# Performance work log

Measured on AMD Instinct MI355X. Metric: run time of the kernel, lower is better.

Reference implementation:

```python
import jax, jax.numpy as jnp
import numpy as np
import jax.scipy.linalg as jsl

N = 20000
E = 320000
IN_FEAT = 128
HID = 128
OUT_FEAT = 64
D = 4            # stalk_dim
K = HID // D     # number of stalks per node
MLP_HID = 64


def setup_inputs() -> dict:
    key = jax.random.key(0)
    ks = jax.random.split(key, 16)
    def lin(kw, kb, fan_in, fan_out):
        s = 1.0 / np.sqrt(fan_in)
        w = jax.random.uniform(kw, (fan_in, fan_out), minval=-s, maxval=s, dtype=jnp.float32)
        b = jax.random.uniform(kb, (fan_out,), minval=-s, maxval=s, dtype=jnp.float32)
        return w, b
    x = jax.random.normal(ks[0], (N, IN_FEAT), dtype=jnp.float32)
    edge_index = jax.random.randint(ks[1], (2, E), 0, N, dtype=jnp.int64)
    lin_in_w, lin_in_b = lin(ks[2], ks[3], IN_FEAT, HID)
    conv0_w1, conv0_b1 = lin(ks[4], ks[5], 2 * HID, MLP_HID)
    conv0_w2, conv0_b2 = lin(ks[6], ks[7], MLP_HID, 2 * D * D)
    conv1_w1, conv1_b1 = lin(ks[8], ks[9], 2 * HID, MLP_HID)
    conv1_w2, conv1_b2 = lin(ks[10], ks[11], MLP_HID, 2 * D * D)
    lin_out_w, lin_out_b = lin(ks[12], ks[13], HID, OUT_FEAT)
    return {
        "x": x, "edge_index": edge_index,
        "lin_in_w": lin_in_w, "lin_in_b": lin_in_b,
        "conv0_w1": conv0_w1, "conv0_b1": conv0_b1,
        "conv0_w2": conv0_w2, "conv0_b2": conv0_b2, "conv0_eps": jnp.float32(0.5),
        "conv1_w1": conv1_w1, "conv1_b1": conv1_b1,
        "conv1_w2": conv1_w2, "conv1_b2": conv1_b2, "conv1_eps": jnp.float32(0.5),
        "lin_out_w": lin_out_w, "lin_out_b": lin_out_b,
    }


def _sheaf_conv(x, row, col, w1, b1, w2, b2, eps):
    # edge gather -> MLP -> skew-symmetric expm -> batched small matmuls -> scatter-add
    x_row = x[row]              # [E, C] source features
    x_col = x[col]              # [E, C] target features
    h = jax.nn.relu(jnp.concatenate([x_row, x_col], axis=-1) @ w1 + b1)
    maps = (h @ w2 + b2).reshape(-1, 2, D, D)        # [E, 2, d, d]
    A = maps - jnp.swapaxes(maps, -1, -2)            # skew-symmetric
    F_e = jax.vmap(jsl.expm)(A.reshape(-1, D, D)).reshape(-1, 2, D, D)
    f_u, f_v = F_e[:, 0], F_e[:, 1]                  # [E, d, d] each
    # PyG default flow: x_i = x[col] (target), x_j = x[row] (source)
    x_i = x_col.reshape(-1, K, D)
    x_j = x_row.reshape(-1, K, D)
    proj_i = jnp.einsum('eab,ekb->eka', f_u, x_i)
    proj_j = jnp.einsum('eab,ekb->eka', f_v, x_j)
    err = proj_i - proj_j
    msg = jnp.einsum('eba,ekb->eka', f_u, err).reshape(-1, K * D)  # f_u^T @ err
    agg = jax.ops.segment_sum(msg, col, num_segments=x.shape[0])   # scatter-add at target
    return x - eps * agg


def reference(x, edge_index, lin_in_w, lin_in_b,
              conv0_w1, conv0_b1, conv0_w2, conv0_b2, conv0_eps,
              conv1_w1, conv1_b1, conv1_w2, conv1_b2, conv1_eps,
              lin_out_w, lin_out_b):
    row, col = edge_index[0], edge_index[1]
    h = x @ lin_in_w + lin_in_b
    h = jax.nn.elu(_sheaf_conv(h, row, col, conv0_w1, conv0_b1, conv0_w2, conv0_b2, conv0_eps))
    h = jax.nn.elu(_sheaf_conv(h, row, col, conv1_w1, conv1_b1, conv1_w2, conv1_b2, conv1_eps))
    return h @ lin_out_w + lin_out_b
```

## Files before the change

### kernel.cpp

```cpp
#include <hip/hip_runtime.h>
#include <math.h>


using short8 = __attribute__((ext_vector_type(8))) short;
using f32x4 = __attribute__((ext_vector_type(4))) float;
typedef unsigned short u16;

__device__ __forceinline__ u16 f2bf(float f) {
  unsigned u = __float_as_uint(f);
  unsigned r = (u + 0x7FFFu + ((u >> 16) & 1u)) >> 16;
  return (u16)r;
}
__device__ __forceinline__ float bf2f(u16 v) {
  return __uint_as_float(((unsigned)v) << 16);
}

__global__ void __launch_bounds__(256) k_prep(const float* __restrict__ x,
    u16* __restrict__ Xb, int* __restrict__ cnt, int n4, int N,
    const float* __restrict__ win, const float* __restrict__ w1a,
    const float* __restrict__ w1b, const float* __restrict__ wout,
    const float* __restrict__ w2a, const float* __restrict__ w2b,
    const float* __restrict__ b1a, const float* __restrict__ b1b,
    u16* __restrict__ WTin, u16* __restrict__ WT1a, u16* __restrict__ WT1b,
    u16* __restrict__ WTout, u16* __restrict__ W2Ta, u16* __restrict__ W2Tb,
    float* __restrict__ B1pa, float* __restrict__ B1pb) {
  int idx = blockIdx.x * 256 + threadIdx.x;
  if (idx < N) cnt[idx] = 0;
  if (idx < n4) {
    float4 v = ((const float4*)x)[idx];
    ushort4 o;
    o.x = f2bf(v.x);
    o.y = f2bf(v.y);
    o.z = f2bf(v.z);
    o.w = f2bf(v.w);
    ((ushort4*)Xb)[idx] = o;
  }
  if (idx < 16384) {
    int o = idx >> 7, i = idx & 127;
    WTin[idx] = f2bf(win[i * 128 + o]);
  } else if (idx < 32768) {
    int j = idx - 16384;
    int o = j >> 7, i = j & 127;
    WT1a[j] = f2bf(o < 64 ? w1a[i * 64 + o] : w1a[(128 + i) * 64 + (o - 64)]);
  } else if (idx < 49152) {
    int j = idx - 32768;
    int o = j >> 7, i = j & 127;
    WT1b[j] = f2bf(o < 64 ? w1b[i * 64 + o] : w1b[(128 + i) * 64 + (o - 64)]);
  } else if (idx < 57344) {
    int j = idx - 49152;
    int o = j >> 7, i = j & 127;
    WTout[j] = f2bf(wout[i * 64 + o]);
  } else if (idx < 59392) {
    int j = idx - 57344;
    int o = j >> 6, k = j & 63;
    W2Ta[j] = f2bf(w2a[k * 32 + o]);
  } else if (idx < 61440) {
    int j = idx - 59392;
    int o = j >> 6, k = j & 63;
    W2Tb[j] = f2bf(w2b[k * 32 + o]);
  } else if (idx < 61568) {
    int j = idx - 61440;
    B1pa[j] = (j < 64) ? 0.f : b1a[j - 64];
  } else if (idx < 61696) {
    int j = idx - 61568;
    B1pb[j] = (j < 64) ? 0.f : b1b[j - 64];
  }
}

__global__ void __launch_bounds__(256) k_gemm_mfma(const u16* __restrict__ Ab,
    const u16* __restrict__ WT, const float* __restrict__ bias,
    float* __restrict__ C, u16* __restrict__ Cb, int N, int P) {
  int t = threadIdx.x;
  int wv = t >> 6, lane = t & 63;
  int row0 = (blockIdx.x << 6) + (wv << 4);
  int cb = blockIdx.y << 4;
  int col = lane & 15, quad = lane >> 4;
  const u16* wrow = WT + (size_t)(cb + col) * 128 + quad * 8;
  short8 b0 = *(const short8*)(wrow);
  short8 b1 = *(const short8*)(wrow + 32);
  short8 b2 = *(const short8*)(wrow + 64);
  short8 b3 = *(const short8*)(wrow + 96);
  float bv = bias ? bias[cb + col] : 0.f;
  const u16* ar = Ab + (size_t)(row0 + col) * 128 + quad * 8;
  short8 a0 = *(const short8*)(ar);
  short8 a1 = *(const short8*)(ar + 32);
  short8 a2 = *(const short8*)(ar + 64);
  short8 a3 = *(const short8*)(ar + 96);
  f32x4 acc = {0.f, 0.f, 0.f, 0.f};
  acc = __builtin_amdgcn_mfma_f32_16x16x32_bf16(a0, b0, acc, 0, 0, 0);
  acc = __builtin_amdgcn_mfma_f32_16x16x32_bf16(a1, b1, acc, 0, 0, 0);
  acc = __builtin_amdgcn_mfma_f32_16x16x32_bf16(a2, b2, acc, 0, 0, 0);
  acc = __builtin_amdgcn_mfma_f32_16x16x32_bf16(a3, b3, acc, 0, 0, 0);
#pragma unroll
  for (int r = 0; r < 4; ++r) {
    int row = row0 + quad * 4 + r;
    if (row < N) {
      float o = acc[r] + bv;
      if (C) C[(size_t)row * P + cb + col] = o;
      if (Cb) Cb[(size_t)row * 128 + cb + col] = f2bf(o);
    }
  }
}

__global__ void __launch_bounds__(256) k_hist(const int* __restrict__ eidx,
                                              int* __restrict__ cnt, int E) {
  int e = blockIdx.x * 256 + threadIdx.x;
  if (e < E) atomicAdd(&cnt[eidx[E + e]], 1);
}

__global__ void __launch_bounds__(256) k_scanA(const int* __restrict__ cnt,
                                               int* __restrict__ bsum, int N) {
  __shared__ int sums[256];
  int b = blockIdx.x, t = threadIdx.x;
  int base = b * 2048 + t * 8;
  int s = 0;
#pragma unroll
  for (int k = 0; k < 8; ++k) {
    int i = base + k;
    if (i < N) s += cnt[i];
  }
  sums[t] = s;
  __syncthreads();
  for (int d = 128; d > 0; d >>= 1) {
    if (t < d) sums[t] += sums[t + d];
    __syncthreads();
  }
  if (t == 0) bsum[b] = sums[0];
}

__global__ void __launch_bounds__(256) k_scanC(const int* __restrict__ cnt,
    const int* __restrict__ bsum, int* __restrict__ ptr,
    int* __restrict__ cursor, int N, int nblocks) {
  __shared__ int sums[256];
  int b = blockIdx.x, t = threadIdx.x;
  int bo = 0;
  for (int k = 0; k < b; ++k) bo += bsum[k];
  int base = b * 2048 + t * 8;
  int vals[8];
  int s = 0;
#pragma unroll
  for (int k = 0; k < 8; ++k) {
    int i = base + k;
    int c = (i < N) ? cnt[i] : 0;
    vals[k] = s;
    s += c;
  }
  sums[t] = s;
  __syncthreads();
  for (int d = 1; d < 256; d <<= 1) {
    int v = (t >= d) ? sums[t - d] : 0;
    __syncthreads();
    sums[t] += v;
    __syncthreads();
  }
  int toff = (t == 0) ? 0 : sums[t - 1];
#pragma unroll
  for (int k = 0; k < 8; ++k) {
    int i = base + k;
    if (i < N) {
      int p = bo + toff + vals[k];
      ptr[i] = p;
      cursor[i] = p;
    }
  }
  if (b == nblocks - 1 && t == 255) ptr[N] = bo + sums[255];
}

__global__ void __launch_bounds__(256) k_fill(const int* __restrict__ eidx,
    int* __restrict__ cursor, int2* __restrict__ adj, int E) {
  int e = blockIdx.x * 256 + threadIdx.x;
  if (e >= E) return;
  int r = eidx[e], c = eidx[E + e];
  int pos = atomicAdd(&cursor[c], 1);
  adj[pos] = make_int2(r, c);
}

__device__ __forceinline__ void so4_expm(const float* __restrict__ m,
                                         float* __restrict__ F) {
  float v1 = m[1] - m[4], v2 = m[2] - m[8], v3 = m[3] - m[12];
  float w1 = m[11] - m[14], w2 = m[13] - m[7], w3 = m[6] - m[9];
  float p1 = 0.5f * (v1 + w1), p2 = 0.5f * (v2 + w2), p3 = 0.5f * (v3 + w3);
  float q1 = 0.5f * (v1 - w1), q2 = 0.5f * (v2 - w2), q3 = 0.5f * (v3 - w3);
  float tp2 = p1 * p1 + p2 * p2 + p3 * p3;
  float tq2 = q1 * q1 + q2 * q2 + q3 * q3;
  float tp = sqrtf(tp2), tq = sqrtf(tq2);
  float cp = __cosf(tp);
  float sp = (tp > 1e-6f) ? (__sinf(tp) / tp) : (1.f - tp2 * (1.f / 6.f));
  float cq = __cosf(tq);
  float sq = (tq > 1e-6f) ? (__sinf(tq) / tq) : (1.f - tq2 * (1.f / 6.f));
  float a1 = sp * p1, a2 = sp * p2, a3 = sp * p3;
  float b1 = sq * q1, b2 = sq * q2, b3 = sq * q3;
  float Rp[16] = {cp,  a1,  a2,  a3,  -a1, cp,  a3,  -a2,
                  -a2, -a3, cp,  a1,  -a3, a2,  -a1, cp};
  float Rq[16] = {cq,  b1,  b2,  b3,  -b1, cq,  -b3, b2,
                  -b2, b3,  cq,  -b1, -b3, -b2, b1,  cq};
#pragma unroll
  for (int a = 0; a < 4; ++a)
#pragma unroll
    for (int b = 0; b < 4; ++b) {
      float s = 0.f;
#pragma unroll
      for (int c = 0; c < 4; ++c) s = fmaf(Rp[a * 4 + c], Rq[c * 4 + b], s);
      F[a * 4 + b] = s;
    }
}

__global__ void __launch_bounds__(64) k_conv(const float* __restrict__ x,
    const u16* __restrict__ xgb, const u16* __restrict__ pqb,
    const u16* __restrict__ W2T, const float* __restrict__ b2,
    const int* __restrict__ ptr, const int2* __restrict__ adj,
    const float* __restrict__ epsp, float* __restrict__ xout,
    u16* __restrict__ xoutb, int N) {
  __shared__ float ms[16 * 44];
  int lane = threadIdx.x;
  int v = blockIdx.x;
  if (v >= N) return;
  int p0 = ptr[v], p1 = ptr[v + 1];
  int el = lane & 15, quad = lane >> 4;
  int a = lane & 3, kb = lane & ~3;
  short8 bf00 = *(const short8*)(W2T + (size_t)el * 64 + quad * 8);
  short8 bf01 = *(const short8*)(W2T + (size_t)el * 64 + 32 + quad * 8);
  short8 bf10 = *(const short8*)(W2T + (size_t)(16 + el) * 64 + quad * 8);
  short8 bf11 = *(const short8*)(W2T + (size_t)(16 + el) * 64 + 32 + quad * 8);
  float b2a = b2[el], b2b = b2[16 + el];
  short8 qv0 = *(const short8*)(pqb + (size_t)v * 128 + 64 + quad * 8);
  short8 qv1 = *(const short8*)(pqb + (size_t)v * 128 + 96 + quad * 8);
  const float* xv = x + (size_t)v * 128;
  float4 xi1 = *(const float4*)(xv + kb);
  float4 xi2 = *(const float4*)(xv + 64 + kb);
  float hv1 = xv[lane], hv2 = xv[64 + lane];
  float s10 = 0.f, s11 = 0.f, s12 = 0.f, s13 = 0.f;
  float acc1 = 0.f, acc2 = 0.f;
  for (int b0 = p0; b0 < p1; b0 += 16) {
    int nb = p1 - b0;
    nb = (nb > 16) ? 16 : nb;
    int ee = b0 + ((el < nb) ? el : (nb - 1));
    int row = adj[ee].x;
    f32x4 c0 = {0.f, 0.f, 0.f, 0.f};
    f32x4 c1 = {0.f, 0.f, 0.f, 0.f};
    {
      short8 pv = *(const short8*)(pqb + (size_t)row * 128 + quad * 8);
      short8 av;
#pragma unroll
      for (int j = 0; j < 8; ++j) {
        float h = bf2f((u16)pv[j]) + bf2f((u16)qv0[j]);
        av[j] = (short)f2bf(fmaxf(h, 0.f));
      }
      c0 = __builtin_amdgcn_mfma_f32_16x16x32_bf16(av, bf00, c0, 0, 0, 0);
      c1 = __builtin_amdgcn_mfma_f32_16x16x32_bf16(av, bf10, c1, 0, 0, 0);
    }
    {
      short8 pv = *(const short8*)(pqb + (size_t)row * 128 + 32 + quad * 8);
      short8 av;
#pragma unroll
      for (int j = 0; j < 8; ++j) {
        float h = bf2f((u16)pv[j]) + bf2f((u16)qv1[j]);
        av[j] = (short)f2bf(fmaxf(h, 0.f));
      }
      c0 = __builtin_amdgcn_mfma_f32_16x16x32_bf16(av, bf01, c0, 0, 0, 0);
      c1 = __builtin_amdgcn_mfma_f32_16x16x32_bf16(av, bf11, c1, 0, 0, 0);
    }
#pragma unroll
    for (int r = 0; r < 4; ++r) {
      ms[(quad * 4 + r) * 44 + el] = c0[r] + b2a;
      ms[(quad * 4 + r) * 44 + 16 + el] = c1[r] + b2b;
    }
    __syncthreads();
    if (lane < 16) {
      float m[32];
      const float* mr = ms + lane * 44;
#pragma unroll
      for (int i = 0; i < 32; ++i) m[i] = mr[i];
      float Fu[16], Fv[16];
      so4_expm(m, Fu);
      so4_expm(m + 16, Fv);
      float* mw = ms + lane * 44;
#pragma unroll
      for (int aa = 0; aa < 4; ++aa)
#pragma unroll
        for (int bb = 0; bb < 4; ++bb) {
          float s1 = 0.f, s2 = 0.f;
#pragma unroll
          for (int cc = 0; cc < 4; ++cc) {
            s1 = fmaf(Fu[cc * 4 + aa], Fu[cc * 4 + bb], s1);
            s2 = fmaf(Fu[cc * 4 + aa], Fv[cc * 4 + bb], s2);
          }
          mw[aa * 4 + bb] = s1;
          mw[16 + aa * 4 + bb] = s2;
        }
    }
    __syncthreads();
    int j = 0;
    for (; j + 1 < nb; j += 2) {
      int r0 = __builtin_amdgcn_readlane(row, j);
      int r1 = __builtin_amdgcn_readlane(row, j + 1);
      float4 am1 = *(const float4*)(ms + j * 44 + a * 4);
      float4 am2 = *(const float4*)(ms + j * 44 + 16 + a * 4);
      float4 bm1 = *(const float4*)(ms + (j + 1) * 44 + a * 4);
      float4 bm2 = *(const float4*)(ms + (j + 1) * 44 + 16 + a * 4);
      ushort4 ya1 = *(const ushort4*)(xgb + (size_t)r0 * 128 + kb);
      ushort4 ya2 = *(const ushort4*)(xgb + (size_t)r0 * 128 + 64 + kb);
      ushort4 yb1 = *(const ushort4*)(xgb + (size_t)r1 * 128 + kb);
      ushort4 yb2 = *(const ushort4*)(xgb + (size_t)r1 * 128 + 64 + kb);
      s10 += am1.x + bm1.x;
      s11 += am1.y + bm1.y;
      s12 += am1.z + bm1.z;
      s13 += am1.w + bm1.w;
      acc1 -= am2.x * bf2f(ya1.x) + am2.y * bf2f(ya1.y) +
              am2.z * bf2f(ya1.z) + am2.w * bf2f(ya1.w);
      acc2 -= am2.x * bf2f(ya2.x) + am2.y * bf2f(ya2.y) +
              am2.z * bf2f(ya2.z) + am2.w * bf2f(ya2.w);
      acc1 -= bm2.x * bf2f(yb1.x) + bm2.y * bf2f(yb1.y) +
              bm2.z * bf2f(yb1.z) + bm2.w * bf2f(yb1.w);
      acc2 -= bm2.x * bf2f(yb2.x) + bm2.y * bf2f(yb2.y) +
              bm2.z * bf2f(yb2.z) + bm2.w * bf2f(yb2.w);
    }
    if (j < nb) {
      int r0 = __builtin_amdgcn_readlane(row, j);
      float4 am1 = *(const float4*)(ms + j * 44 + a * 4);
      float4 am2 = *(const float4*)(ms + j * 44 + 16 + a * 4);
      ushort4 ya1 = *(const ushort4*)(xgb + (size_t)r0 * 128 + kb);
      ushort4 ya2 = *(const ushort4*)(xgb + (size_t)r0 * 128 + 64 + kb);
      s10 += am1.x;
      s11 += am1.y;
      s12 += am1.z;
      s13 += am1.w;
      acc1 -= am2.x * bf2f(ya1.x) + am2.y * bf2f(ya1.y) +
              am2.z * bf2f(ya1.z) + am2.w * bf2f(ya1.w);
      acc2 -= am2.x * bf2f(ya2.x) + am2.y * bf2f(ya2.y) +
              am2.z * bf2f(ya2.z) + am2.w * bf2f(ya2.w);
    }
    __syncthreads();
  }
  acc1 += s10 * xi1.x + s11 * xi1.y + s12 * xi1.z + s13 * xi1.w;
  acc2 += s10 * xi2.x + s11 * xi2.y + s12 * xi2.z + s13 * xi2.w;
  float eps = *epsp;
  float r1 = hv1 - eps * acc1;
  float r2 = hv2 - eps * acc2;
  r1 = (r1 > 0.f) ? r1 : expm1f(r1);
  r2 = (r2 > 0.f) ? r2 : expm1f(r2);
  xout[(size_t)v * 128 + lane] = r1;
  xout[(size_t)v * 128 + 64 + lane] = r2;
  xoutb[(size_t)v * 128 + lane] = f2bf(r1);
  xoutb[(size_t)v * 128 + 64 + lane] = f2bf(r2);
}

extern "C" void kernel_launch(void* const* d_in, const int* in_sizes, int n_in,
                              void* d_out, int out_size, void* d_ws,
                              size_t ws_size, hipStream_t stream) {
  const float* x = (const float*)d_in[0];
  const int* eidx = (const int*)d_in[1];
  const float* lin_in_w = (const float*)d_in[2];
  const float* lin_in_b = (const float*)d_in[3];
  const float* c0w1 = (const float*)d_in[4];
  const float* c0b1 = (const float*)d_in[5];
  const float* c0w2 = (const float*)d_in[6];
  const float* c0b2 = (const float*)d_in[7];
  const float* c0eps = (const float*)d_in[8];
  const float* c1w1 = (const float*)d_in[9];
  const float* c1b1 = (const float*)d_in[10];
  const float* c1w2 = (const float*)d_in[11];
  const float* c1b2 = (const float*)d_in[12];
  const float* c1eps = (const float*)d_in[13];
  const float* lout_w = (const float*)d_in[14];
  const float* lout_b = (const float*)d_in[15];
  float* out = (float*)d_out;

  int N = in_sizes[0] / 128;
  int E = in_sizes[1] / 2;
  int Npad = N + 64;

  char* ws = (char*)d_ws;
  size_t szH = (size_t)N * 128 * 4;
  size_t szHb = (size_t)Npad * 128 * 2;
  float* H = (float*)ws;
  float* H2 = (float*)(ws + szH);
  u16* Xb = (u16*)(ws + 2 * szH);
  u16* Hb = (u16*)(ws + 2 * szH + szHb);
  u16* H2b = (u16*)(ws + 2 * szH + 2 * szHb);
  u16* PQb = (u16*)(ws + 2 * szH + 3 * szHb);
  u16* WTin = (u16*)(ws + 2 * szH + 4 * szHb);
  u16* WT1a = WTin + 16384;
  u16* WT1b = WT1a + 16384;
  u16* WTout = WT1b + 16384;
  u16* W2Ta = WTout + 8192;
  u16* W2Tb = W2Ta + 2048;
  float* B1pa = (float*)(W2Tb + 2048);
  float* B1pb = B1pa + 128;
  char* ip = (char*)(B1pb + 128);
  int* cnt = (int*)ip;
  int* ptr = (int*)(ip + 4 * (size_t)(N + 64));
  int* cursor = (int*)(ip + 8 * (size_t)(N + 64));
  int2* adj = (int2*)(ip + 12 * (size_t)(N + 64));
  int* bsum = (int*)(ip + 12 * (size_t)(N + 64) + 8 * (size_t)E);

  dim3 blk(256);
  int gN = (N + 63) / 64;
  int gE = (E + 255) / 256;
  int nsb = (N + 2047) / 2048;

  k_prep<<<(N * 32 + 255) / 256, blk, 0, stream>>>(
      x, Xb, cnt, N * 32, N, lin_in_w, c0w1, c1w1, lout_w, c0w2, c1w2, c0b1,
      c1b1, WTin, WT1a, WT1b, WTout, W2Ta, W2Tb, B1pa, B1pb);
  k_hist<<<gE, blk, 0, stream>>>(eidx, cnt, E);
  k_scanA<<<nsb, blk, 0, stream>>>(cnt, bsum, N);
  k_scanC<<<nsb, blk, 0, stream>>>(cnt, bsum, ptr, cursor, N, nsb);
  k_fill<<<gE, blk, 0, stream>>>(eidx, cursor, adj, E);

  k_gemm_mfma<<<dim3(gN, 8), blk, 0, stream>>>(Xb, WTin, lin_in_b, H, Hb, N,
                                               128);

  float* cur = H;
  float* nxt = H2;
  u16* curb = Hb;
  u16* nxtb = H2b;
  for (int layer = 0; layer < 2; ++layer) {
    const u16* wt1 = layer ? WT1b : WT1a;
    const u16* w2t = layer ? W2Tb : W2Ta;
    const float* b1p = layer ? B1pb : B1pa;
    const float* b2 = layer ? c1b2 : c0b2;
    const float* ep = layer ? c1eps : c0eps;
    k_gemm_mfma<<<dim3(gN, 8), blk, 0, stream>>>(curb, wt1, b1p, nullptr, PQb,
                                                 N, 128);
    k_conv<<<N, dim3(64), 0, stream>>>(cur, curb, PQb, w2t, b2, ptr, adj, ep,
                                       nxt, nxtb, N);
    float* tf = cur; cur = nxt; nxt = tf;
    u16* tb = curb; curb = nxtb; nxtb = tb;
  }

  k_gemm_mfma<<<dim3(gN, 4), blk, 0, stream>>>(curb, WTout, lout_b, out,
                                               nullptr, N, 64);
}
```

Measured before the change: 283.7 us.

## Pack four node-waves per conv block with wave-local sync, fp32 neighbor gather

The conv kernel now runs four nodes per 256-thread block, one wave each, with a private shared-memory slice per wave. Block-wide __syncthreads is replaced by a wave-local lgkmcnt wait, which is enough because each wave only touches its own slice. The per-edge ReLU/bf16 conversion now uses packed v_cvt_pk_bf16_f32 with the q-part pre-converted to float. Neighbor features are gathered from the fp32 copy instead of the bf16 copy, which doubles the bytes gathered per edge in exchange for precision and fewer conversions.

```diff
diff --git a/kernel.cpp b/kernel.cpp
--- a/kernel.cpp
+++ b/kernel.cpp
@@ -13,6 +13,12 @@
 }
 __device__ __forceinline__ float bf2f(u16 v) {
   return __uint_as_float(((unsigned)v) << 16);
+}
+
+__device__ __forceinline__ void wave_sync() {
+  __builtin_amdgcn_sched_barrier(0);
+  asm volatile("s_waitcnt lgkmcnt(0)" ::: "memory");
+  __builtin_amdgcn_sched_barrier(0);
 }
 
 __global__ void __launch_bounds__(256) k_prep(const float* __restrict__ x,
@@ -205,16 +211,18 @@
     }
 }
 
-__global__ void __launch_bounds__(64) k_conv(const float* __restrict__ x,
-    const u16* __restrict__ xgb, const u16* __restrict__ pqb,
+__global__ void __launch_bounds__(256) k_conv(const float* __restrict__ x,
+    const u16* __restrict__ pqb,
     const u16* __restrict__ W2T, const float* __restrict__ b2,
     const int* __restrict__ ptr, const int2* __restrict__ adj,
     const float* __restrict__ epsp, float* __restrict__ xout,
     u16* __restrict__ xoutb, int N) {
-  __shared__ float ms[16 * 44];
-  int lane = threadIdx.x;
-  int v = blockIdx.x;
+  __shared__ float msAll[4][16 * 44];
+  int lane = threadIdx.x & 63;
+  int wv = threadIdx.x >> 6;
+  int v = (blockIdx.x << 2) + wv;
   if (v >= N) return;
+  float* ms = msAll[wv];
   int p0 = ptr[v], p1 = ptr[v + 1];
   int el = lane & 15, quad = lane >> 4;
   int a = lane & 3, kb = lane & ~3;
@@ -225,6 +233,12 @@
   float b2a = b2[el], b2b = b2[16 + el];
   short8 qv0 = *(const short8*)(pqb + (size_t)v * 128 + 64 + quad * 8);
   short8 qv1 = *(const short8*)(pqb + (size_t)v * 128 + 96 + quad * 8);
+  float qf0[8], qf1[8];
+#pragma unroll
+  for (int j = 0; j < 8; ++j) {
+    qf0[j] = bf2f((u16)qv0[j]);
+    qf1[j] = bf2f((u16)qv1[j]);
+  }
   const float* xv = x + (size_t)v * 128;
   float4 xi1 = *(const float4*)(xv + kb);
   float4 xi2 = *(const float4*)(xv + 64 + kb);
@@ -240,32 +254,38 @@
     f32x4 c1 = {0.f, 0.f, 0.f, 0.f};
     {
       short8 pv = *(const short8*)(pqb + (size_t)row * 128 + quad * 8);
-      short8 av;
-#pragma unroll
-      for (int j = 0; j < 8; ++j) {
-        float h = bf2f((u16)pv[j]) + bf2f((u16)qv0[j]);
-        av[j] = (short)f2bf(fmaxf(h, 0.f));
+      union { short8 s; unsigned u[4]; } av;
+#pragma unroll
+      for (int j2 = 0; j2 < 4; ++j2) {
+        float h0 = fmaxf(bf2f((u16)pv[2 * j2]) + qf0[2 * j2], 0.f);
+        float h1 = fmaxf(bf2f((u16)pv[2 * j2 + 1]) + qf0[2 * j2 + 1], 0.f);
+        unsigned r;
+        asm("v_cvt_pk_bf16_f32 %0, %1, %2" : "=v"(r) : "v"(h0), "v"(h1));
+        av.u[j2] = r;
       }
-      c0 = __builtin_amdgcn_mfma_f32_16x16x32_bf16(av, bf00, c0, 0, 0, 0);
-      c1 = __builtin_amdgcn_mfma_f32_16x16x32_bf16(av, bf10, c1, 0, 0, 0);
+      c0 = __builtin_amdgcn_mfma_f32_16x16x32_bf16(av.s, bf00, c0, 0, 0, 0);
+      c1 = __builtin_amdgcn_mfma_f32_16x16x32_bf16(av.s, bf10, c1, 0, 0, 0);
     }
     {
       short8 pv = *(const short8*)(pqb + (size_t)row * 128 + 32 + quad * 8);
-      short8 av;
-#pragma unroll
-      for (int j = 0; j < 8; ++j) {
-        float h = bf2f((u16)pv[j]) + bf2f((u16)qv1[j]);
-        av[j] = (short)f2bf(fmaxf(h, 0.f));
+      union { short8 s; unsigned u[4]; } av;
+#pragma unroll
+      for (int j2 = 0; j2 < 4; ++j2) {
+        float h0 = fmaxf(bf2f((u16)pv[2 * j2]) + qf1[2 * j2], 0.f);
+        float h1 = fmaxf(bf2f((u16)pv[2 * j2 + 1]) + qf1[2 * j2 + 1], 0.f);
+        unsigned r;
+        asm("v_cvt_pk_bf16_f32 %0, %1, %2" : "=v"(r) : "v"(h0), "v"(h1));
+        av.u[j2] = r;
       }
-      c0 = __builtin_amdgcn_mfma_f32_16x16x32_bf16(av, bf01, c0, 0, 0, 0);
-      c1 = __builtin_amdgcn_mfma_f32_16x16x32_bf16(av, bf11, c1, 0, 0, 0);
+      c0 = __builtin_amdgcn_mfma_f32_16x16x32_bf16(av.s, bf01, c0, 0, 0, 0);
+      c1 = __builtin_amdgcn_mfma_f32_16x16x32_bf16(av.s, bf11, c1, 0, 0, 0);
     }
 #pragma unroll
     for (int r = 0; r < 4; ++r) {
       ms[(quad * 4 + r) * 44 + el] = c0[r] + b2a;
       ms[(quad * 4 + r) * 44 + 16 + el] = c1[r] + b2b;
     }
-    __syncthreads();
+    wave_sync();
     if (lane < 16) {
       float m[32];
       const float* mr = ms + lane * 44;
@@ -289,7 +309,7 @@
           mw[16 + aa * 4 + bb] = s2;
         }
     }
-    __syncthreads();
+    wave_sync();
     int j = 0;
     for (; j + 1 < nb; j += 2) {
       int r0 = __builtin_amdgcn_readlane(row, j);
@@ -298,39 +318,33 @@
       float4 am2 = *(const float4*)(ms + j * 44 + 16 + a * 4);
       float4 bm1 = *(const float4*)(ms + (j + 1) * 44 + a * 4);
       float4 bm2 = *(const float4*)(ms + (j + 1) * 44 + 16 + a * 4);
-      ushort4 ya1 = *(const ushort4*)(xgb + (size_t)r0 * 128 + kb);
-      ushort4 ya2 = *(const ushort4*)(xgb + (size_t)r0 * 128 + 64 + kb);
-      ushort4 yb1 = *(const ushort4*)(xgb + (size_t)r1 * 128 + kb);
-      ushort4 yb2 = *(const ushort4*)(xgb + (size_t)r1 * 128 + 64 + kb);
+      float4 ya1 = *(const float4*)(x + (size_t)r0 * 128 + kb);
+      float4 ya2 = *(const float4*)(x + (size_t)r0 * 128 + 64 + kb);
+      float4 yb1 = *(const float4*)(x + (size_t)r1 * 128 + kb);
+      float4 yb2 = *(const float4*)(x + (size_t)r1 * 128 + 64 + kb);
       s10 += am1.x + bm1.x;
       s11 += am1.y + bm1.y;
       s12 += am1.z + bm1.z;
       s13 += am1.w + bm1.w;
-      acc1 -= am2.x * bf2f(ya1.x) + am2.y * bf2f(ya1.y) +
-              am2.z * bf2f(ya1.z) + am2.w * bf2f(ya1.w);
-      acc2 -= am2.x * bf2f(ya2.x) + am2.y * bf2f(ya2.y) +
-              am2.z * bf2f(ya2.z) + am2.w * bf2f(ya2.w);
-      acc1 -= bm2.x * bf2f(yb1.x) + bm2.y * bf2f(yb1.y) +
-              bm2.z * bf2f(yb1.z) + bm2.w * bf2f(yb1.w);
-      acc2 -= bm2.x * bf2f(yb2.x) + bm2.y * bf2f(yb2.y) +
-              bm2.z * bf2f(yb2.z) + bm2.w * bf2f(yb2.w);
+      acc1 -= am2.x * ya1.x + am2.y * ya1.y + am2.z * ya1.z + am2.w * ya1.w;
+      acc2 -= am2.x * ya2.x + am2.y * ya2.y + am2.z * ya2.z + am2.w * ya2.w;
+      acc1 -= bm2.x * yb1.x + bm2.y * yb1.y + bm2.z * yb1.z + bm2.w * yb1.w;
+      acc2 -= bm2.x * yb2.x + bm2.y * yb2.y + bm2.z * yb2.z + bm2.w * yb2.w;
     }
     if (j < nb) {
       int r0 = __builtin_amdgcn_readlane(row, j);
       float4 am1 = *(const float4*)(ms + j * 44 + a * 4);
       float4 am2 = *(const float4*)(ms + j * 44 + 16 + a * 4);
-      ushort4 ya1 = *(const ushort4*)(xgb + (size_t)r0 * 128 + kb);
-      ushort4 ya2 = *(const ushort4*)(xgb + (size_t)r0 * 128 + 64 + kb);
+      float4 ya1 = *(const float4*)(x + (size_t)r0 * 128 + kb);
+      float4 ya2 = *(const float4*)(x + (size_t)r0 * 128 + 64 + kb);
       s10 += am1.x;
       s11 += am1.y;
       s12 += am1.z;
       s13 += am1.w;
-      acc1 -= am2.x * bf2f(ya1.x) + am2.y * bf2f(ya1.y) +
-              am2.z * bf2f(ya1.z) + am2.w * bf2f(ya1.w);
-      acc2 -= am2.x * bf2f(ya2.x) + am2.y * bf2f(ya2.y) +
-              am2.z * bf2f(ya2.z) + am2.w * bf2f(ya2.w);
-    }
-    __syncthreads();
+      acc1 -= am2.x * ya1.x + am2.y * ya1.y + am2.z * ya1.z + am2.w * ya1.w;
+      acc2 -= am2.x * ya2.x + am2.y * ya2.y + am2.z * ya2.z + am2.w * ya2.w;
+    }
+    wave_sync();
   }
   acc1 += s10 * xi1.x + s11 * xi1.y + s12 * xi1.z + s13 * xi1.w;
   acc2 += s10 * xi2.x + s11 * xi2.y + s12 * xi2.z + s13 * xi2.w;
@@ -397,6 +411,7 @@
   dim3 blk(256);
   int gN = (N + 63) / 64;
   int gE = (E + 255) / 256;
+  int gC = (N + 3) / 4;
   int nsb = (N + 2047) / 2048;
 
   k_prep<<<(N * 32 + 255) / 256, blk, 0, stream>>>(
@@ -422,8 +437,8 @@
     const float* ep = layer ? c1eps : c0eps;
     k_gemm_mfma<<<dim3(gN, 8), blk, 0, stream>>>(curb, wt1, b1p, nullptr, PQb,
                                                  N, 128);
-    k_conv<<<N, dim3(64), 0, stream>>>(cur, curb, PQb, w2t, b2, ptr, adj, ep,
-                                       nxt, nxtb, N);
+    k_conv<<<gC, blk, 0, stream>>>(cur, PQb, w2t, b2, ptr, adj, ep, nxt, nxtb,
+                                   N);
     float* tf = cur; cur = nxt; nxt = tf;
     u16* tb = curb; curb = nxtb; nxtb = tb;
   }
```

After: 322.5 us. 13.7% more time.
